# Optimization experiments

Measured on AMD Instinct MI355X. Metric: run time of the kernel, lower is better.

Reference implementation:

```python
import jax, jax.numpy as jnp
import numpy as np

B_G = 16        # number of point clouds
N_PER = 32768   # points per cloud (equal -> no padding)
T = B_G * N_PER
CIN = 16
D = 32          # global_dim
H = 4           # num_heads
HD = D // H
L = 2           # layers
EPS_LN = 1e-5
EPS_Z = 1e-6


def setup_inputs() -> dict:
    key = jax.random.key(0)
    ks = jax.random.split(key, 32)
    r = lambda i, shape, s: (jax.random.normal(ks[i], shape, dtype=jnp.float32) * s)
    inp = {
        "x": r(0, (T, CIN), 1.0),
        "pos": r(1, (T, 3), 1.0),
        "batch": (jnp.arange(T, dtype=jnp.int32) // N_PER),
        "w_in": r(2, (CIN, D), CIN ** -0.5),
        "b_in": r(3, (D,), 0.02),
        "w_pos": r(4, (3, D), 3 ** -0.5),
        "b_pos": r(5, (D,), 0.02),
        "wq": r(6, (L, D, D), D ** -0.5),
        "bq": r(7, (L, D), 0.02),
        "wk": r(8, (L, D, D), D ** -0.5),
        "bk": r(9, (L, D), 0.02),
        "wv": r(10, (L, D, D), D ** -0.5),
        "bv": r(11, (L, D), 0.02),
        "wo": r(12, (L, D, D), D ** -0.5),
        "bo": r(13, (L, D), 0.02),
        "g1": jnp.ones((L, D), jnp.float32),
        "be1": jnp.zeros((L, D), jnp.float32),
        "w1": r(14, (L, D, 2 * D), D ** -0.5),
        "bf1": r(15, (L, 2 * D), 0.02),
        "w2": r(16, (L, 2 * D, D), (2 * D) ** -0.5),
        "bf2": r(17, (L, D), 0.02),
        "g2": jnp.ones((L, D), jnp.float32),
        "be2": jnp.zeros((L, D), jnp.float32),
    }
    return inp


def _layernorm(h, g, b):
    mu = jnp.mean(h, axis=-1, keepdims=True)
    var = jnp.mean(jnp.square(h - mu), axis=-1, keepdims=True)
    return (h - mu) * jax.lax.rsqrt(var + EPS_LN) * g + b


def _linear_attn(h, wq, bq, wk, bk, wv, bv, wo, bo):
    B, N, C = h.shape
    def heads(w, b):
        return (h @ w + b).reshape(B, N, H, HD).transpose(0, 2, 1, 3)  # [B,H,N,hd]
    q = jax.nn.elu(heads(wq, bq)) + 1.0   # ELU feature map phi(.)
    k = jax.nn.elu(heads(wk, bk)) + 1.0
    v = heads(wv, bv)
    kv = jnp.einsum("bhnd,bhne->bhde", k, v)            # O(N) KV summary
    ksum = k.sum(axis=2)                                   # [B,H,hd]
    z = 1.0 / (jnp.einsum("bhnd,bhd->bhn", q, ksum) + EPS_Z)
    out = jnp.einsum("bhnd,bhde->bhne", q, kv) * z[..., None]
    out = out.transpose(0, 2, 1, 3).reshape(B, N, C)
    return out @ wo + bo


def reference(x, pos, batch, w_in, b_in, w_pos, b_pos, wq, bq, wk, bk, wv, bv,
              wo, bo, g1, be1, w1, bf1, w2, bf2, g2, be2):
    # to_dense_batch: batch is sorted; compute per-point index within its segment
    counts = jax.ops.segment_sum(jnp.ones((T,), jnp.int32), batch, num_segments=B_G)
    starts = jnp.concatenate([jnp.zeros((1,), jnp.int32), jnp.cumsum(counts)[:-1]])
    idx = jnp.arange(T, dtype=jnp.int32) - starts[batch]
    x_dense = jnp.zeros((B_G, N_PER, CIN), x.dtype).at[batch, idx].set(x)
    pos_dense = jnp.zeros((B_G, N_PER, 3), pos.dtype).at[batch, idx].set(pos)

    h = (x_dense @ w_in + b_in) + (pos_dense @ w_pos + b_pos)  # [B,N,D]
    for l in range(L):
        h = _layernorm(h + _linear_attn(h, wq[l], bq[l], wk[l], bk[l],
                                        wv[l], bv[l], wo[l], bo[l]), g1[l], be1[l])
        ffn = jax.nn.relu(h @ w1[l] + bf1[l]) @ w2[l] + bf2[l]
        h = _layernorm(h + ffn, g2[l], be2[l])
    return h[batch, idx]  # back to [T, D] (h[mask])
```

## Files before the change

### kernel.cpp

```cpp
#include <hip/hip_runtime.h>

#define KVSZ 288
#define EPS_LN 1e-5f
#define EPS_Z  1e-6f

typedef __attribute__((ext_vector_type(8))) short bf16x8;
typedef __attribute__((ext_vector_type(4))) float f32x4;

#define MFMA(a, b, c) __builtin_amdgcn_mfma_f32_16x16x32_bf16(a, b, c, 0, 0, 0)

#define PWE 0
#define LBASE(l) (1024 + (l) * 8192)
#define PQ 0
#define PO 1024
#define P1 2048
#define P2 4096
#define PK 6144
#define PV 7168

__device__ __forceinline__ unsigned short f2bf(float f) {
  union { float f; unsigned u; } x; x.f = f;
  unsigned r = x.u + 0x7fff + ((x.u >> 16) & 1);
  return (unsigned short)(r >> 16);
}

__device__ __forceinline__ unsigned pkbf(float a, float b) {
#if __has_builtin(__builtin_amdgcn_cvt_pk_bf16_f32)
  typedef __attribute__((ext_vector_type(2))) __bf16 bf16x2_t;
  bf16x2_t v = __builtin_amdgcn_cvt_pk_bf16_f32(a, b);
  return __builtin_bit_cast(unsigned, v);
#else
  return (unsigned)f2bf(a) | ((unsigned)f2bf(b) << 16);
#endif
}

__device__ __forceinline__ float bfu(unsigned short s) {
  union { float f; unsigned u; } x; x.u = ((unsigned)s) << 16; return x.f;
}

__device__ __forceinline__ void lds_fence() { asm volatile("s_waitcnt lgkmcnt(0)" ::: "memory"); }
__device__ __forceinline__ float phi(float x) { return x > 0.f ? x + 1.f : __expf(x); }

__device__ __forceinline__ int perm32(int kp) {
  return ((kp & 4) << 2) | (((kp >> 3) << 2) + (kp & 3));
}

__device__ __forceinline__ bf16x8 bbuild(f32x4 lo, f32x4 hi) {
  union { bf16x8 v; unsigned u[4]; } cv;
  cv.u[0] = pkbf(lo[0], lo[1]); cv.u[1] = pkbf(lo[2], lo[3]);
  cv.u[2] = pkbf(hi[0], hi[1]); cv.u[3] = pkbf(hi[2], hi[3]);
  return cv.v;
}

__device__ __forceinline__ void stage_a32(unsigned short* dst, const float* __restrict__ W,
                                          int N, int tid) {
  for (int i = tid; i < 32 * N; i += 256) {
    int n = i >> 5, kp = i & 31;
    dst[i] = f2bf(W[perm32(kp) * N + n]);
  }
}
__device__ __forceinline__ void stage_a64(unsigned short* dst, const float* __restrict__ W,
                                          int tid) {
  for (int i = tid; i < 64 * 32; i += 256) {
    int n = i >> 6, kp = i & 63;
    int kl = ((kp >> 5) << 5) + perm32(kp & 31);
    dst[i] = f2bf(W[kl * 32 + n]);
  }
}

__device__ __forceinline__ void make_kvm(bf16x8& A0, bf16x8& A1,
                                         const float* __restrict__ kvg,
                                         int quad, int m) {
  union { bf16x8 v; unsigned short s[8]; unsigned u[4]; } a, b;
  a.u[0] = a.u[1] = a.u[2] = a.u[3] = 0u;
  b.u[0] = b.u[1] = b.u[2] = b.u[3] = 0u;
  if ((quad >> 1) == (m >> 3)) {
    int h0 = m >> 3, e7 = m & 7, dq = (quad & 1) * 4;
    const float* p0 = kvg + h0 * 64 + dq * 8 + e7;
    const float* p1 = kvg + (2 + h0) * 64 + dq * 8 + e7;
    a.s[0] = f2bf(p0[0]);  a.s[1] = f2bf(p0[8]);
    a.s[2] = f2bf(p0[16]); a.s[3] = f2bf(p0[24]);
    b.s[4] = f2bf(p1[0]);  b.s[5] = f2bf(p1[8]);
    b.s[6] = f2bf(p1[16]); b.s[7] = f2bf(p1[24]);
  }
  A0 = a.v; A1 = b.v;
}

__device__ __forceinline__ void ln_t(f32x4& a0, f32x4& a1, float4 g0, float4 g1,
                                     float4 b0, float4 b1) {
  float s = a0[0] + a0[1] + a0[2] + a0[3] + a1[0] + a1[1] + a1[2] + a1[3];
  s += __shfl_xor(s, 16); s += __shfl_xor(s, 32);
  float mu = s * (1.f / 32.f);
  float vv = 0.f;
#pragma unroll
  for (int r = 0; r < 4; r++) {
    a0[r] -= mu; a1[r] -= mu;
    vv += a0[r] * a0[r] + a1[r] * a1[r];
  }
  vv += __shfl_xor(vv, 16); vv += __shfl_xor(vv, 32);
  float rstd = rsqrtf(vv * (1.f / 32.f) + EPS_LN);
  a0[0] = a0[0] * rstd * g0.x + b0.x; a0[1] = a0[1] * rstd * g0.y + b0.y;
  a0[2] = a0[2] * rstd * g0.z + b0.z; a0[3] = a0[3] * rstd * g0.w + b0.w;
  a1[0] = a1[0] * rstd * g1.x + b1.x; a1[1] = a1[1] * rstd * g1.y + b1.y;
  a1[2] = a1[2] * rstd * g1.z + b1.z; a1[3] = a1[3] * rstd * g1.w + b1.w;
}

__device__ __forceinline__ void layer_core_g(
    f32x4 (&hc0)[4], f32x4 (&hc1)[4], const unsigned short* __restrict__ pwl,
    const float* __restrict__ kvg, int quad, int m,
    const float* __restrict__ bq, const float* __restrict__ bo,
    const float* __restrict__ g1, const float* __restrict__ be1,
    const float* __restrict__ bf1, const float* __restrict__ bf2,
    const float* __restrict__ g2, const float* __restrict__ be2) {
  const int k0 = quad * 8, q4 = quad * 4;
  {
    const bf16x8 wqA0 = *(const bf16x8*)(pwl + PQ + m * 32 + k0);
    const bf16x8 wqA1 = *(const bf16x8*)(pwl + PQ + (16 + m) * 32 + k0);
    const bf16x8 woA0 = *(const bf16x8*)(pwl + PO + m * 32 + k0);
    const bf16x8 woA1 = *(const bf16x8*)(pwl + PO + (16 + m) * 32 + k0);
    bf16x8 kvA0, kvA1;
    make_kvm(kvA0, kvA1, kvg, quad, m);
    const float4 bq0 = *(const float4*)(bq + q4), bq1 = *(const float4*)(bq + 16 + q4);
    const float4 bo0 = *(const float4*)(bo + q4), bo1 = *(const float4*)(bo + 16 + q4);
    const float4 g10 = *(const float4*)(g1 + q4), g11 = *(const float4*)(g1 + 16 + q4);
    const float4 e10 = *(const float4*)(be1 + q4), e11 = *(const float4*)(be1 + 16 + q4);
    const float4 ks0 = *(const float4*)(kvg + 256 + q4);
    const float4 ks1 = *(const float4*)(kvg + 272 + q4);
#pragma unroll
    for (int mt = 0; mt < 4; mt++) {
      bf16x8 hB = bbuild(hc0[mt], hc1[mt]);
      f32x4 q0 = {bq0.x, bq0.y, bq0.z, bq0.w};
      f32x4 q1 = {bq1.x, bq1.y, bq1.z, bq1.w};
      q0 = MFMA(wqA0, hB, q0);
      q1 = MFMA(wqA1, hB, q1);
#pragma unroll
      for (int r = 0; r < 4; r++) { q0[r] = phi(q0[r]); q1[r] = phi(q1[r]); }
      bf16x8 qB = bbuild(q0, q1);
      f32x4 zz = {0.f, 0.f, 0.f, 0.f};
      f32x4 at0 = MFMA(kvA0, qB, zz);
      f32x4 at1 = MFMA(kvA1, qB, zz);
      float p0 = q0[0] * ks0.x + q0[1] * ks0.y + q0[2] * ks0.z + q0[3] * ks0.w;
      float p1 = q1[0] * ks1.x + q1[1] * ks1.y + q1[2] * ks1.z + q1[3] * ks1.w;
      p0 += __shfl_xor(p0, 16);
      p1 += __shfl_xor(p1, 16);
      float z0 = 1.f / (p0 + EPS_Z), z1 = 1.f / (p1 + EPS_Z);
      bf16x8 aB;
      {
        union { bf16x8 v; unsigned u[4]; } cv;
        cv.u[0] = pkbf(at0[0] * z0, at0[1] * z0); cv.u[1] = pkbf(at0[2] * z0, at0[3] * z0);
        cv.u[2] = pkbf(at1[0] * z1, at1[1] * z1); cv.u[3] = pkbf(at1[2] * z1, at1[3] * z1);
        aB = cv.v;
      }
      f32x4 h0 = hc0[mt], h1 = hc1[mt];
      h0[0] += bo0.x; h0[1] += bo0.y; h0[2] += bo0.z; h0[3] += bo0.w;
      h1[0] += bo1.x; h1[1] += bo1.y; h1[2] += bo1.z; h1[3] += bo1.w;
      h0 = MFMA(woA0, aB, h0);
      h1 = MFMA(woA1, aB, h1);
      ln_t(h0, h1, g10, g11, e10, e11);
      hc0[mt] = h0; hc1[mt] = h1;
    }
  }
  {
    bf16x8 w1A[4]; float4 b1f[4];
#pragma unroll
    for (int nt = 0; nt < 4; nt++) {
      w1A[nt] = *(const bf16x8*)(pwl + P1 + (nt * 16 + m) * 32 + k0);
      b1f[nt] = *(const float4*)(bf1 + nt * 16 + q4);
    }
    const bf16x8 w2L0 = *(const bf16x8*)(pwl + P2 + m * 64 + k0);
    const bf16x8 w2H0 = *(const bf16x8*)(pwl + P2 + m * 64 + 32 + k0);
    const bf16x8 w2L1 = *(const bf16x8*)(pwl + P2 + (16 + m) * 64 + k0);
    const bf16x8 w2H1 = *(const bf16x8*)(pwl + P2 + (16 + m) * 64 + 32 + k0);
    const float4 b20 = *(const float4*)(bf2 + q4), b21 = *(const float4*)(bf2 + 16 + q4);
    const float4 g20 = *(const float4*)(g2 + q4), g21 = *(const float4*)(g2 + 16 + q4);
    const float4 e20 = *(const float4*)(be2 + q4), e21 = *(const float4*)(be2 + 16 + q4);
#pragma unroll
    for (int mt = 0; mt < 4; mt++) {
      bf16x8 hB = bbuild(hc0[mt], hc1[mt]);
      f32x4 hd[4];
#pragma unroll
      for (int nt = 0; nt < 4; nt++) {
        f32x4 ini = {b1f[nt].x, b1f[nt].y, b1f[nt].z, b1f[nt].w};
        hd[nt] = MFMA(w1A[nt], hB, ini);
#pragma unroll
        for (int r = 0; r < 4; r++) hd[nt][r] = fmaxf(hd[nt][r], 0.f);
      }
      bf16x8 fL = bbuild(hd[0], hd[1]);
      bf16x8 fH = bbuild(hd[2], hd[3]);
      f32x4 o0 = hc0[mt], o1 = hc1[mt];
      o0[0] += b20.x; o0[1] += b20.y; o0[2] += b20.z; o0[3] += b20.w;
      o1[0] += b21.x; o1[1] += b21.y; o1[2] += b21.z; o1[3] += b21.w;
      o0 = MFMA(w2L0, fL, o0);
      o0 = MFMA(w2H0, fH, o0);
      o1 = MFMA(w2L1, fL, o1);
      o1 = MFMA(w2H1, fH, o1);
      ln_t(o0, o1, g20, g21, e20, e21);
      hc0[mt] = o0; hc1[mt] = o1;
    }
  }
}

__device__ __forceinline__ void kv_stage_g(
    const f32x4 (&hc0)[4], const f32x4 (&hc1)[4], unsigned short* tw,
    const unsigned short* __restrict__ pwk, const unsigned short* __restrict__ pwv,
    float* blk, int quad, int m,
    const float* __restrict__ bk, const float* __restrict__ bv) {
  const int k0 = quad * 8, q4 = quad * 4;
  unsigned short* Tk = tw;
  unsigned short* Tv = tw + 1280;
  const bf16x8 wkA0 = *(const bf16x8*)(pwk + m * 32 + k0);
  const bf16x8 wkA1 = *(const bf16x8*)(pwk + (16 + m) * 32 + k0);
  const bf16x8 wvA0 = *(const bf16x8*)(pwv + m * 32 + k0);
  const bf16x8 wvA1 = *(const bf16x8*)(pwv + (16 + m) * 32 + k0);
  const float4 bk0 = *(const float4*)(bk + q4), bk1 = *(const float4*)(bk + 16 + q4);
  const float4 bv0 = *(const float4*)(bv + q4), bv1 = *(const float4*)(bv + 16 + q4);
  f32x4 accA = {0.f, 0.f, 0.f, 0.f}, accB = {0.f, 0.f, 0.f, 0.f};
  f32x4 ksa0 = {0.f, 0.f, 0.f, 0.f}, ksa1 = {0.f, 0.f, 0.f, 0.f};
#pragma unroll
  for (int ch = 0; ch < 2; ch++) {
#pragma unroll
    for (int mtl = 0; mtl < 2; mtl++) {
      int mt = ch * 2 + mtl;
      bf16x8 hB = bbuild(hc0[mt], hc1[mt]);
      f32x4 kn0 = {bk0.x, bk0.y, bk0.z, bk0.w};
      f32x4 kn1 = {bk1.x, bk1.y, bk1.z, bk1.w};
      f32x4 vn0 = {bv0.x, bv0.y, bv0.z, bv0.w};
      f32x4 vn1 = {bv1.x, bv1.y, bv1.z, bv1.w};
      kn0 = MFMA(wkA0, hB, kn0);
      kn1 = MFMA(wkA1, hB, kn1);
      vn0 = MFMA(wvA0, hB, vn0);
      vn1 = MFMA(wvA1, hB, vn1);
      int cb = mtl * 16 + m;
#pragma unroll
      for (int r = 0; r < 4; r++) {
        kn0[r] = phi(kn0[r]); kn1[r] = phi(kn1[r]);
        ksa0[r] += kn0[r];    ksa1[r] += kn1[r];
        Tk[(q4 + r) * 40 + cb]      = f2bf(kn0[r]);
        Tk[(16 + q4 + r) * 40 + cb] = f2bf(kn1[r]);
        Tv[(q4 + r) * 40 + cb]      = f2bf(vn0[r]);
        Tv[(16 + q4 + r) * 40 + cb] = f2bf(vn1[r]);
      }
    }
    lds_fence();
    bf16x8 akL = *(const bf16x8*)(Tk + m * 40 + k0);
    bf16x8 akH = *(const bf16x8*)(Tk + (16 + m) * 40 + k0);
    bf16x8 avL = *(const bf16x8*)(Tv + m * 40 + k0);
    bf16x8 avH = *(const bf16x8*)(Tv + (16 + m) * 40 + k0);
    accA = MFMA(akL, avL, accA);
    accB = MFMA(akH, avH, accB);
    lds_fence();
  }
#pragma unroll
  for (int r = 0; r < 4; r++) {
    float v0 = ksa0[r], v1 = ksa1[r];
    v0 += __shfl_xor(v0, 1); v0 += __shfl_xor(v0, 2); v0 += __shfl_xor(v0, 4); v0 += __shfl_xor(v0, 8);
    v1 += __shfl_xor(v1, 1); v1 += __shfl_xor(v1, 2); v1 += __shfl_xor(v1, 4); v1 += __shfl_xor(v1, 8);
    if (m == 0) {
      atomicAdd(&blk[256 + q4 + r], v0);
      atomicAdd(&blk[272 + q4 + r], v1);
    }
  }
  if ((quad >> 1) == (m >> 3)) {
    int h0 = quad >> 1, h1 = 2 + (quad >> 1), e = m & 7;
#pragma unroll
    for (int r = 0; r < 4; r++) {
      int d = (q4 + r) & 7;
      atomicAdd(&blk[h0 * 64 + d * 8 + e], accA[r]);
      atomicAdd(&blk[h1 * 64 + d * 8 + e], accB[r]);
    }
  }
}

__global__ __launch_bounds__(256) void k_prep(
    const float* __restrict__ w_in, const float* __restrict__ w_pos,
    const float* __restrict__ wq, const float* __restrict__ wk,
    const float* __restrict__ wv, const float* __restrict__ wo,
    const float* __restrict__ w1, const float* __restrict__ w2,
    unsigned short* __restrict__ pw) {
  const int tid = threadIdx.x;
  for (int i = tid; i < 1024; i += 256) {
    int n = i >> 5, k = i & 31;
    float v = k < 16 ? w_in[k * 32 + n] : (k < 19 ? w_pos[(k - 16) * 32 + n] : 0.f);
    pw[PWE + i] = f2bf(v);
  }
  for (int l = 0; l < 2; l++) {
    unsigned short* b = pw + LBASE(l);
    stage_a32(b + PQ, wq + l * 1024, 32, tid);
    stage_a32(b + PO, wo + l * 1024, 32, tid);
    stage_a32(b + P1, w1 + l * 2048, 64, tid);
    stage_a64(b + P2, w2 + l * 2048, tid);
    stage_a32(b + PK, wk + l * 1024, 32, tid);
    stage_a32(b + PV, wv + l * 1024, 32, tid);
  }
}

template <int H16>
__global__ __launch_bounds__(256) void k_embed(
    const float* __restrict__ x, const float* __restrict__ pos,
    const float* __restrict__ b_in, const float* __restrict__ b_pos,
    const float* __restrict__ bk, const float* __restrict__ bv,
    const unsigned short* __restrict__ pw, unsigned short* __restrict__ hb,
    float* __restrict__ hf, float* __restrict__ gkv) {
  __shared__ __align__(16) unsigned short tiles[4 * 2560];
  __shared__ float blk[KVSZ];
  const int tid = threadIdx.x;
  const int wv_ = tid >> 6, lane = tid & 63, quad = lane >> 4, m = lane & 15;
  unsigned short* tw = tiles + wv_ * 2560;
  const int cloud = blockIdx.x >> 7;
  const int wbase = blockIdx.x * 256 + wv_ * 64;
  const int k0 = quad * 8, q4 = quad * 4;
  for (int i = tid; i < KVSZ; i += 256) blk[i] = 0.f;
  __syncthreads();
  const bf16x8 weA0 = *(const bf16x8*)(pw + PWE + m * 32 + k0);
  const bf16x8 weA1 = *(const bf16x8*)(pw + PWE + (16 + m) * 32 + k0);
  float4 bi0, bi1;
  {
    float4 a = *(const float4*)(b_in + q4), b = *(const float4*)(b_pos + q4);
    bi0 = make_float4(a.x + b.x, a.y + b.y, a.z + b.z, a.w + b.w);
    float4 c = *(const float4*)(b_in + 16 + q4), d = *(const float4*)(b_pos + 16 + q4);
    bi1 = make_float4(c.x + d.x, c.y + d.y, c.z + d.z, c.w + d.w);
  }
  f32x4 hc0[4], hc1[4];
#pragma unroll
  for (int mt = 0; mt < 4; mt++) {
    int p = wbase + mt * 16 + m;
    union { bf16x8 v; unsigned u[4]; } xb;
    xb.u[0] = xb.u[1] = xb.u[2] = xb.u[3] = 0;
    if (quad < 2) {
      const float4* xp = (const float4*)(x + (size_t)p * 16 + quad * 8);
      float4 t0 = xp[0], t1 = xp[1];
      xb.u[0] = pkbf(t0.x, t0.y); xb.u[1] = pkbf(t0.z, t0.w);
      xb.u[2] = pkbf(t1.x, t1.y); xb.u[3] = pkbf(t1.z, t1.w);
    } else if (quad == 2) {
      const float* pp = pos + (size_t)p * 3;
      xb.u[0] = pkbf(pp[0], pp[1]); xb.u[1] = pkbf(pp[2], 0.f);
    }
    f32x4 i0 = {bi0.x, bi0.y, bi0.z, bi0.w};
    f32x4 i1 = {bi1.x, bi1.y, bi1.z, bi1.w};
    hc0[mt] = MFMA(weA0, xb.v, i0);
    hc1[mt] = MFMA(weA1, xb.v, i1);
    if (H16) {
      *(bf16x8*)(hb + ((size_t)p * 32 + quad * 8)) = bbuild(hc0[mt], hc1[mt]);
    } else {
      float* hp = hf + (size_t)p * 32;
      *(float4*)(hp + q4)      = make_float4(hc0[mt][0], hc0[mt][1], hc0[mt][2], hc0[mt][3]);
      *(float4*)(hp + 16 + q4) = make_float4(hc1[mt][0], hc1[mt][1], hc1[mt][2], hc1[mt][3]);
    }
  }
  kv_stage_g(hc0, hc1, tw, pw + LBASE(0) + PK, pw + LBASE(0) + PV, blk, quad, m, bk, bv);
  __syncthreads();
  float* g = gkv + cloud * KVSZ;
  for (int i = tid; i < KVSZ; i += 256) atomicAdd(&g[i], blk[i]);
}

template <int H16>
__global__ __launch_bounds__(256) void k_mid(
    const float* __restrict__ bq, const float* __restrict__ bo,
    const float* __restrict__ g1, const float* __restrict__ be1,
    const float* __restrict__ bf1, const float* __restrict__ bf2,
    const float* __restrict__ g2, const float* __restrict__ be2,
    const float* __restrict__ bkn, const float* __restrict__ bvn,
    const unsigned short* __restrict__ pw, const float* __restrict__ kv_in,
    float* __restrict__ gkv_out, unsigned short* __restrict__ hb,
    float* __restrict__ hf) {
  __shared__ __align__(16) unsigned short tiles[4 * 2560];
  __shared__ float blk[KVSZ];
  const int tid = threadIdx.x;
  const int wv_ = tid >> 6, lane = tid & 63, quad = lane >> 4, m = lane & 15;
  unsigned short* tw = tiles + wv_ * 2560;
  const int cloud = blockIdx.x >> 7;
  const int wbase = blockIdx.x * 256 + wv_ * 64;
  const int q4 = quad * 4;
  for (int i = tid; i < KVSZ; i += 256) blk[i] = 0.f;
  __syncthreads();
  f32x4 hc0[4], hc1[4];
#pragma unroll
  for (int mt = 0; mt < 4; mt++) {
    int p = wbase + mt * 16 + m;
    if (H16) {
      bf16x8 hv = *(const bf16x8*)(hb + ((size_t)p * 32 + quad * 8));
#pragma unroll
      for (int r = 0; r < 4; r++) {
        hc0[mt][r] = bfu((unsigned short)hv[r]);
        hc1[mt][r] = bfu((unsigned short)hv[4 + r]);
      }
    } else {
      const float* hp = hf + (size_t)p * 32;
      float4 lo = *(const float4*)(hp + q4);
      float4 hi = *(const float4*)(hp + 16 + q4);
      hc0[mt][0] = lo.x; hc0[mt][1] = lo.y; hc0[mt][2] = lo.z; hc0[mt][3] = lo.w;
      hc1[mt][0] = hi.x; hc1[mt][1] = hi.y; hc1[mt][2] = hi.z; hc1[mt][3] = hi.w;
    }
  }
  layer_core_g(hc0, hc1, pw + LBASE(0), kv_in + cloud * KVSZ, quad, m,
               bq, bo, g1, be1, bf1, bf2, g2, be2);
#pragma unroll
  for (int mt = 0; mt < 4; mt++) {
    int p = wbase + mt * 16 + m;
    if (H16) {
      *(bf16x8*)(hb + ((size_t)p * 32 + quad * 8)) = bbuild(hc0[mt], hc1[mt]);
    } else {
      float* hp = hf + (size_t)p * 32;
      *(float4*)(hp + q4)      = make_float4(hc0[mt][0], hc0[mt][1], hc0[mt][2], hc0[mt][3]);
      *(float4*)(hp + 16 + q4) = make_float4(hc1[mt][0], hc1[mt][1], hc1[mt][2], hc1[mt][3]);
    }
  }
  kv_stage_g(hc0, hc1, tw, pw + LBASE(1) + PK, pw + LBASE(1) + PV, blk, quad, m,
             bkn, bvn);
  __syncthreads();
  float* g = gkv_out + cloud * KVSZ;
  for (int i = tid; i < KVSZ; i += 256) atomicAdd(&g[i], blk[i]);
}

template <int H16>
__global__ __launch_bounds__(256) void k_last(
    const float* __restrict__ bq, const float* __restrict__ bo,
    const float* __restrict__ g1, const float* __restrict__ be1,
    const float* __restrict__ bf1, const float* __restrict__ bf2,
    const float* __restrict__ g2, const float* __restrict__ be2,
    const unsigned short* __restrict__ pw, const float* __restrict__ kv_in,
    const unsigned short* __restrict__ hb, float* __restrict__ out) {
  const int tid = threadIdx.x;
  const int wv_ = tid >> 6, lane = tid & 63, quad = lane >> 4, m = lane & 15;
  const int cloud = blockIdx.x >> 7;
  const int wbase = blockIdx.x * 256 + wv_ * 64;
  const int q4 = quad * 4;
  f32x4 hc0[4], hc1[4];
#pragma unroll
  for (int mt = 0; mt < 4; mt++) {
    int p = wbase + mt * 16 + m;
    if (H16) {
      bf16x8 hv = *(const bf16x8*)(hb + ((size_t)p * 32 + quad * 8));
#pragma unroll
      for (int r = 0; r < 4; r++) {
        hc0[mt][r] = bfu((unsigned short)hv[r]);
        hc1[mt][r] = bfu((unsigned short)hv[4 + r]);
      }
    } else {
      const float* hp = out + (size_t)p * 32;
      float4 lo = *(const float4*)(hp + q4);
      float4 hi = *(const float4*)(hp + 16 + q4);
      hc0[mt][0] = lo.x; hc0[mt][1] = lo.y; hc0[mt][2] = lo.z; hc0[mt][3] = lo.w;
      hc1[mt][0] = hi.x; hc1[mt][1] = hi.y; hc1[mt][2] = hi.z; hc1[mt][3] = hi.w;
    }
  }
  layer_core_g(hc0, hc1, pw + LBASE(1), kv_in + cloud * KVSZ, quad, m,
               bq, bo, g1, be1, bf1, bf2, g2, be2);
#pragma unroll
  for (int mt = 0; mt < 4; mt++) {
    int p = wbase + mt * 16 + m;
    float* hp = out + (size_t)p * 32;
    *(float4*)(hp + q4)      = make_float4(hc0[mt][0], hc0[mt][1], hc0[mt][2], hc0[mt][3]);
    *(float4*)(hp + 16 + q4) = make_float4(hc1[mt][0], hc1[mt][1], hc1[mt][2], hc1[mt][3]);
  }
}

extern "C" void kernel_launch(void* const* d_in, const int* in_sizes, int n_in,
                              void* d_out, int out_size, void* d_ws, size_t ws_size,
                              hipStream_t stream) {
  (void)in_sizes; (void)n_in; (void)out_size;
  const float* x     = (const float*)d_in[0];
  const float* pos   = (const float*)d_in[1];
  const float* w_in  = (const float*)d_in[3];
  const float* b_in  = (const float*)d_in[4];
  const float* w_pos = (const float*)d_in[5];
  const float* b_pos = (const float*)d_in[6];
  const float* wq  = (const float*)d_in[7];
  const float* bq  = (const float*)d_in[8];
  const float* wk  = (const float*)d_in[9];
  const float* bk  = (const float*)d_in[10];
  const float* wv  = (const float*)d_in[11];
  const float* bv  = (const float*)d_in[12];
  const float* wo  = (const float*)d_in[13];
  const float* bo  = (const float*)d_in[14];
  const float* g1  = (const float*)d_in[15];
  const float* be1 = (const float*)d_in[16];
  const float* w1  = (const float*)d_in[17];
  const float* bf1 = (const float*)d_in[18];
  const float* w2  = (const float*)d_in[19];
  const float* bf2 = (const float*)d_in[20];
  const float* g2  = (const float*)d_in[21];
  const float* be2 = (const float*)d_in[22];
  float* out = (float*)d_out;
  float* kvbuf = (float*)d_ws;
  unsigned short* pw = (unsigned short*)((char*)d_ws + 40960);
  unsigned short* hb = (unsigned short*)((char*)d_ws + 131072);
  const size_t need = 131072ull + 524288ull * 32ull * 2ull;
  const bool h16 = ws_size >= need;

  hipMemsetAsync(kvbuf, 0, 2 * 16 * KVSZ * sizeof(float), stream);
  k_prep<<<dim3(1), dim3(256), 0, stream>>>(w_in, w_pos, wq, wk, wv, wo, w1, w2, pw);
  dim3 grid(2048), block(256);
  if (h16) {
    k_embed<1><<<grid, block, 0, stream>>>(x, pos, b_in, b_pos, bk, bv, pw, hb, out, kvbuf);
    k_mid<1><<<grid, block, 0, stream>>>(bq, bo, g1, be1, bf1, bf2, g2, be2,
                                         bk + 32, bv + 32, pw, kvbuf,
                                         kvbuf + 16 * KVSZ, hb, out);
    k_last<1><<<grid, block, 0, stream>>>(bq + 32, bo + 32, g1 + 32, be1 + 32,
                                          bf1 + 64, bf2 + 32, g2 + 32, be2 + 32,
                                          pw, kvbuf + 16 * KVSZ, hb, out);
  } else {
    k_embed<0><<<grid, block, 0, stream>>>(x, pos, b_in, b_pos, bk, bv, pw, hb, out, kvbuf);
    k_mid<0><<<grid, block, 0, stream>>>(bq, bo, g1, be1, bf1, bf2, g2, be2,
                                         bk + 32, bv + 32, pw, kvbuf,
                                         kvbuf + 16 * KVSZ, hb, out);
    k_last<0><<<grid, block, 0, stream>>>(bq + 32, bo + 32, g1 + 32, be1 + 32,
                                          bf1 + 64, bf2 + 32, g2 + 32, be2 + 32,
                                          pw, kvbuf + 16 * KVSZ, hb, out);
  }
}
```

Before: 267.2 us.

## Stage layer weights and block-diagonal KV matrix in LDS, reuse bf16 fragments

Each block now copies the bf16 layer weights, the KV summary matrix (built once per block as a block-diagonal bf16 tile) and the k-sum vector into shared memory. Per-lane MFMA operands are then read from LDS instead of global memory, and the per-lane make_kvm construction is removed. The bf16 h fragments are also kept and reused for the Q/K/V MFMAs rather than rebuilt from fp32. The cost is extra LDS per block, which may lower occupancy, plus one cooperative staging pass and a sync at the start of each block.

```diff
diff --git a/kernel.cpp b/kernel.cpp
--- a/kernel.cpp
+++ b/kernel.cpp
@@ -68,22 +68,14 @@
   }
 }
 
-__device__ __forceinline__ void make_kvm(bf16x8& A0, bf16x8& A1,
-                                         const float* __restrict__ kvg,
-                                         int quad, int m) {
-  union { bf16x8 v; unsigned short s[8]; unsigned u[4]; } a, b;
-  a.u[0] = a.u[1] = a.u[2] = a.u[3] = 0u;
-  b.u[0] = b.u[1] = b.u[2] = b.u[3] = 0u;
-  if ((quad >> 1) == (m >> 3)) {
-    int h0 = m >> 3, e7 = m & 7, dq = (quad & 1) * 4;
-    const float* p0 = kvg + h0 * 64 + dq * 8 + e7;
-    const float* p1 = kvg + (2 + h0) * 64 + dq * 8 + e7;
-    a.s[0] = f2bf(p0[0]);  a.s[1] = f2bf(p0[8]);
-    a.s[2] = f2bf(p0[16]); a.s[3] = f2bf(p0[24]);
-    b.s[4] = f2bf(p1[0]);  b.s[5] = f2bf(p1[8]);
-    b.s[6] = f2bf(p1[16]); b.s[7] = f2bf(p1[24]);
-  }
-  A0 = a.v; A1 = b.v;
+__device__ __forceinline__ void stage_kvm_lds(unsigned short* dst,
+                                              const float* __restrict__ kvg, int tid) {
+  for (int i = tid; i < 1024; i += 256) {
+    int e = i >> 5, kp = i & 31;
+    int d = perm32(kp);
+    float v = ((d >> 3) == (e >> 3)) ? kvg[(e >> 3) * 64 + (d & 7) * 8 + (e & 7)] : 0.f;
+    dst[i] = f2bf(v);
+  }
 }
 
 __device__ __forceinline__ void ln_t(f32x4& a0, f32x4& a1, float4 g0, float4 g1,
@@ -105,34 +97,34 @@
   a1[2] = a1[2] * rstd * g1.z + b1.z; a1[3] = a1[3] * rstd * g1.w + b1.w;
 }
 
-__device__ __forceinline__ void layer_core_g(
-    f32x4 (&hc0)[4], f32x4 (&hc1)[4], const unsigned short* __restrict__ pwl,
-    const float* __restrict__ kvg, int quad, int m,
+__device__ __forceinline__ void layer_core_l(
+    f32x4 (&hc0)[4], f32x4 (&hc1)[4], const bf16x8 (&hBp)[4],
+    const unsigned short* lw, const unsigned short* kvm, const float* kss,
+    int quad, int m,
     const float* __restrict__ bq, const float* __restrict__ bo,
     const float* __restrict__ g1, const float* __restrict__ be1,
     const float* __restrict__ bf1, const float* __restrict__ bf2,
     const float* __restrict__ g2, const float* __restrict__ be2) {
   const int k0 = quad * 8, q4 = quad * 4;
   {
-    const bf16x8 wqA0 = *(const bf16x8*)(pwl + PQ + m * 32 + k0);
-    const bf16x8 wqA1 = *(const bf16x8*)(pwl + PQ + (16 + m) * 32 + k0);
-    const bf16x8 woA0 = *(const bf16x8*)(pwl + PO + m * 32 + k0);
-    const bf16x8 woA1 = *(const bf16x8*)(pwl + PO + (16 + m) * 32 + k0);
-    bf16x8 kvA0, kvA1;
-    make_kvm(kvA0, kvA1, kvg, quad, m);
+    const bf16x8 wqA0 = *(const bf16x8*)(lw + PQ + m * 32 + k0);
+    const bf16x8 wqA1 = *(const bf16x8*)(lw + PQ + (16 + m) * 32 + k0);
+    const bf16x8 woA0 = *(const bf16x8*)(lw + PO + m * 32 + k0);
+    const bf16x8 woA1 = *(const bf16x8*)(lw + PO + (16 + m) * 32 + k0);
+    const bf16x8 kvA0 = *(const bf16x8*)(kvm + m * 32 + k0);
+    const bf16x8 kvA1 = *(const bf16x8*)(kvm + (16 + m) * 32 + k0);
     const float4 bq0 = *(const float4*)(bq + q4), bq1 = *(const float4*)(bq + 16 + q4);
     const float4 bo0 = *(const float4*)(bo + q4), bo1 = *(const float4*)(bo + 16 + q4);
     const float4 g10 = *(const float4*)(g1 + q4), g11 = *(const float4*)(g1 + 16 + q4);
     const float4 e10 = *(const float4*)(be1 + q4), e11 = *(const float4*)(be1 + 16 + q4);
-    const float4 ks0 = *(const float4*)(kvg + 256 + q4);
-    const float4 ks1 = *(const float4*)(kvg + 272 + q4);
+    const float4 ks0 = *(const float4*)(kss + q4);
+    const float4 ks1 = *(const float4*)(kss + 16 + q4);
 #pragma unroll
     for (int mt = 0; mt < 4; mt++) {
-      bf16x8 hB = bbuild(hc0[mt], hc1[mt]);
       f32x4 q0 = {bq0.x, bq0.y, bq0.z, bq0.w};
       f32x4 q1 = {bq1.x, bq1.y, bq1.z, bq1.w};
-      q0 = MFMA(wqA0, hB, q0);
-      q1 = MFMA(wqA1, hB, q1);
+      q0 = MFMA(wqA0, hBp[mt], q0);
+      q1 = MFMA(wqA1, hBp[mt], q1);
 #pragma unroll
       for (int r = 0; r < 4; r++) { q0[r] = phi(q0[r]); q1[r] = phi(q1[r]); }
       bf16x8 qB = bbuild(q0, q1);
@@ -164,13 +156,13 @@
     bf16x8 w1A[4]; float4 b1f[4];
 #pragma unroll
     for (int nt = 0; nt < 4; nt++) {
-      w1A[nt] = *(const bf16x8*)(pwl + P1 + (nt * 16 + m) * 32 + k0);
+      w1A[nt] = *(const bf16x8*)(lw + P1 + (nt * 16 + m) * 32 + k0);
       b1f[nt] = *(const float4*)(bf1 + nt * 16 + q4);
     }
-    const bf16x8 w2L0 = *(const bf16x8*)(pwl + P2 + m * 64 + k0);
-    const bf16x8 w2H0 = *(const bf16x8*)(pwl + P2 + m * 64 + 32 + k0);
-    const bf16x8 w2L1 = *(const bf16x8*)(pwl + P2 + (16 + m) * 64 + k0);
-    const bf16x8 w2H1 = *(const bf16x8*)(pwl + P2 + (16 + m) * 64 + 32 + k0);
+    const bf16x8 w2L0 = *(const bf16x8*)(lw + P2 + m * 64 + k0);
+    const bf16x8 w2H0 = *(const bf16x8*)(lw + P2 + m * 64 + 32 + k0);
+    const bf16x8 w2L1 = *(const bf16x8*)(lw + P2 + (16 + m) * 64 + k0);
+    const bf16x8 w2H1 = *(const bf16x8*)(lw + P2 + (16 + m) * 64 + 32 + k0);
     const float4 b20 = *(const float4*)(bf2 + q4), b21 = *(const float4*)(bf2 + 16 + q4);
     const float4 g20 = *(const float4*)(g2 + q4), g21 = *(const float4*)(g2 + 16 + q4);
     const float4 e20 = *(const float4*)(be2 + q4), e21 = *(const float4*)(be2 + 16 + q4);
@@ -200,18 +192,18 @@
   }
 }
 
-__device__ __forceinline__ void kv_stage_g(
-    const f32x4 (&hc0)[4], const f32x4 (&hc1)[4], unsigned short* tw,
-    const unsigned short* __restrict__ pwk, const unsigned short* __restrict__ pwv,
+__device__ __forceinline__ void kv_stage_l(
+    const bf16x8 (&hBp)[4], unsigned short* tw,
+    const unsigned short* lwK, const unsigned short* lwV,
     float* blk, int quad, int m,
     const float* __restrict__ bk, const float* __restrict__ bv) {
   const int k0 = quad * 8, q4 = quad * 4;
   unsigned short* Tk = tw;
   unsigned short* Tv = tw + 1280;
-  const bf16x8 wkA0 = *(const bf16x8*)(pwk + m * 32 + k0);
-  const bf16x8 wkA1 = *(const bf16x8*)(pwk + (16 + m) * 32 + k0);
-  const bf16x8 wvA0 = *(const bf16x8*)(pwv + m * 32 + k0);
-  const bf16x8 wvA1 = *(const bf16x8*)(pwv + (16 + m) * 32 + k0);
+  const bf16x8 wkA0 = *(const bf16x8*)(lwK + m * 32 + k0);
+  const bf16x8 wkA1 = *(const bf16x8*)(lwK + (16 + m) * 32 + k0);
+  const bf16x8 wvA0 = *(const bf16x8*)(lwV + m * 32 + k0);
+  const bf16x8 wvA1 = *(const bf16x8*)(lwV + (16 + m) * 32 + k0);
   const float4 bk0 = *(const float4*)(bk + q4), bk1 = *(const float4*)(bk + 16 + q4);
   const float4 bv0 = *(const float4*)(bv + q4), bv1 = *(const float4*)(bv + 16 + q4);
   f32x4 accA = {0.f, 0.f, 0.f, 0.f}, accB = {0.f, 0.f, 0.f, 0.f};
@@ -221,15 +213,14 @@
 #pragma unroll
     for (int mtl = 0; mtl < 2; mtl++) {
       int mt = ch * 2 + mtl;
-      bf16x8 hB = bbuild(hc0[mt], hc1[mt]);
       f32x4 kn0 = {bk0.x, bk0.y, bk0.z, bk0.w};
       f32x4 kn1 = {bk1.x, bk1.y, bk1.z, bk1.w};
       f32x4 vn0 = {bv0.x, bv0.y, bv0.z, bv0.w};
       f32x4 vn1 = {bv1.x, bv1.y, bv1.z, bv1.w};
-      kn0 = MFMA(wkA0, hB, kn0);
-      kn1 = MFMA(wkA1, hB, kn1);
-      vn0 = MFMA(wvA0, hB, vn0);
-      vn1 = MFMA(wvA1, hB, vn1);
+      kn0 = MFMA(wkA0, hBp[mt], kn0);
+      kn1 = MFMA(wkA1, hBp[mt], kn1);
+      vn0 = MFMA(wvA0, hBp[mt], vn0);
+      vn1 = MFMA(wvA1, hBp[mt], vn1);
       int cb = mtl * 16 + m;
 #pragma unroll
       for (int r = 0; r < 4; r++) {
@@ -301,6 +292,7 @@
     const float* __restrict__ bk, const float* __restrict__ bv,
     const unsigned short* __restrict__ pw, unsigned short* __restrict__ hb,
     float* __restrict__ hf, float* __restrict__ gkv) {
+  __shared__ __align__(16) unsigned short lws[3072];
   __shared__ __align__(16) unsigned short tiles[4 * 2560];
   __shared__ float blk[KVSZ];
   const int tid = threadIdx.x;
@@ -309,10 +301,16 @@
   const int cloud = blockIdx.x >> 7;
   const int wbase = blockIdx.x * 256 + wv_ * 64;
   const int k0 = quad * 8, q4 = quad * 4;
+  for (int j = tid; j < 384; j += 256) {
+    int i = j * 8;
+    const unsigned short* src = (i < 1024) ? (pw + PWE + i)
+                                           : (pw + LBASE(0) + PK + (i - 1024));
+    *(bf16x8*)(lws + i) = *(const bf16x8*)src;
+  }
   for (int i = tid; i < KVSZ; i += 256) blk[i] = 0.f;
   __syncthreads();
-  const bf16x8 weA0 = *(const bf16x8*)(pw + PWE + m * 32 + k0);
-  const bf16x8 weA1 = *(const bf16x8*)(pw + PWE + (16 + m) * 32 + k0);
+  const bf16x8 weA0 = *(const bf16x8*)(lws + m * 32 + k0);
+  const bf16x8 weA1 = *(const bf16x8*)(lws + (16 + m) * 32 + k0);
   float4 bi0, bi1;
   {
     float4 a = *(const float4*)(b_in + q4), b = *(const float4*)(b_pos + q4);
@@ -320,7 +318,7 @@
     float4 c = *(const float4*)(b_in + 16 + q4), d = *(const float4*)(b_pos + 16 + q4);
     bi1 = make_float4(c.x + d.x, c.y + d.y, c.z + d.z, c.w + d.w);
   }
-  f32x4 hc0[4], hc1[4];
+  bf16x8 fr[4];
 #pragma unroll
   for (int mt = 0; mt < 4; mt++) {
     int p = wbase + mt * 16 + m;
@@ -337,17 +335,18 @@
     }
     f32x4 i0 = {bi0.x, bi0.y, bi0.z, bi0.w};
     f32x4 i1 = {bi1.x, bi1.y, bi1.z, bi1.w};
-    hc0[mt] = MFMA(weA0, xb.v, i0);
-    hc1[mt] = MFMA(weA1, xb.v, i1);
+    f32x4 h0 = MFMA(weA0, xb.v, i0);
+    f32x4 h1 = MFMA(weA1, xb.v, i1);
+    fr[mt] = bbuild(h0, h1);
     if (H16) {
-      *(bf16x8*)(hb + ((size_t)p * 32 + quad * 8)) = bbuild(hc0[mt], hc1[mt]);
+      *(bf16x8*)(hb + ((size_t)p * 32 + quad * 8)) = fr[mt];
     } else {
       float* hp = hf + (size_t)p * 32;
-      *(float4*)(hp + q4)      = make_float4(hc0[mt][0], hc0[mt][1], hc0[mt][2], hc0[mt][3]);
-      *(float4*)(hp + 16 + q4) = make_float4(hc1[mt][0], hc1[mt][1], hc1[mt][2], hc1[mt][3]);
-    }
-  }
-  kv_stage_g(hc0, hc1, tw, pw + LBASE(0) + PK, pw + LBASE(0) + PV, blk, quad, m, bk, bv);
+      *(float4*)(hp + q4)      = make_float4(h0[0], h0[1], h0[2], h0[3]);
+      *(float4*)(hp + 16 + q4) = make_float4(h1[0], h1[1], h1[2], h1[3]);
+    }
+  }
+  kv_stage_l(fr, tw, lws + 1024, lws + 2048, blk, quad, m, bk, bv);
   __syncthreads();
   float* g = gkv + cloud * KVSZ;
   for (int i = tid; i < KVSZ; i += 256) atomicAdd(&g[i], blk[i]);
@@ -363,6 +362,9 @@
     const unsigned short* __restrict__ pw, const float* __restrict__ kv_in,
     float* __restrict__ gkv_out, unsigned short* __restrict__ hb,
     float* __restrict__ hf) {
+  __shared__ __align__(16) unsigned short lws[8192];
+  __shared__ __align__(16) unsigned short kvm[1024];
+  __shared__ __align__(16) float kss[32];
   __shared__ __align__(16) unsigned short tiles[4 * 2560];
   __shared__ float blk[KVSZ];
   const int tid = threadIdx.x;
@@ -371,18 +373,28 @@
   const int cloud = blockIdx.x >> 7;
   const int wbase = blockIdx.x * 256 + wv_ * 64;
   const int q4 = quad * 4;
+  const float* kvg = kv_in + cloud * KVSZ;
+  for (int j = tid; j < 1024; j += 256) {
+    int i = j * 8;
+    const unsigned short* src = (i < 6144) ? (pw + LBASE(0) + i)
+                                           : (pw + LBASE(1) + PK + (i - 6144));
+    *(bf16x8*)(lws + i) = *(const bf16x8*)src;
+  }
+  stage_kvm_lds(kvm, kvg, tid);
+  if (tid < 32) kss[tid] = kvg[256 + tid];
   for (int i = tid; i < KVSZ; i += 256) blk[i] = 0.f;
   __syncthreads();
   f32x4 hc0[4], hc1[4];
+  bf16x8 fr[4];
 #pragma unroll
   for (int mt = 0; mt < 4; mt++) {
     int p = wbase + mt * 16 + m;
     if (H16) {
-      bf16x8 hv = *(const bf16x8*)(hb + ((size_t)p * 32 + quad * 8));
+      fr[mt] = *(const bf16x8*)(hb + ((size_t)p * 32 + quad * 8));
 #pragma unroll
       for (int r = 0; r < 4; r++) {
-        hc0[mt][r] = bfu((unsigned short)hv[r]);
-        hc1[mt][r] = bfu((unsigned short)hv[4 + r]);
+        hc0[mt][r] = bfu((unsigned short)fr[mt][r]);
+        hc1[mt][r] = bfu((unsigned short)fr[mt][4 + r]);
       }
     } else {
       const float* hp = hf + (size_t)p * 32;
@@ -390,23 +402,24 @@
       float4 hi = *(const float4*)(hp + 16 + q4);
       hc0[mt][0] = lo.x; hc0[mt][1] = lo.y; hc0[mt][2] = lo.z; hc0[mt][3] = lo.w;
       hc1[mt][0] = hi.x; hc1[mt][1] = hi.y; hc1[mt][2] = hi.z; hc1[mt][3] = hi.w;
-    }
-  }
-  layer_core_g(hc0, hc1, pw + LBASE(0), kv_in + cloud * KVSZ, quad, m,
+      fr[mt] = bbuild(hc0[mt], hc1[mt]);
+    }
+  }
+  layer_core_l(hc0, hc1, fr, lws, kvm, kss, quad, m,
                bq, bo, g1, be1, bf1, bf2, g2, be2);
 #pragma unroll
   for (int mt = 0; mt < 4; mt++) {
     int p = wbase + mt * 16 + m;
+    fr[mt] = bbuild(hc0[mt], hc1[mt]);
     if (H16) {
-      *(bf16x8*)(hb + ((size_t)p * 32 + quad * 8)) = bbuild(hc0[mt], hc1[mt]);
+      *(bf16x8*)(hb + ((size_t)p * 32 + quad * 8)) = fr[mt];
     } else {
       float* hp = hf + (size_t)p * 32;
       *(float4*)(hp + q4)      = make_float4(hc0[mt][0], hc0[mt][1], hc0[mt][2], hc0[mt][3]);
       *(float4*)(hp + 16 + q4) = make_float4(hc1[mt][0], hc1[mt][1], hc1[mt][2], hc1[mt][3]);
     }
   }
-  kv_stage_g(hc0, hc1, tw, pw + LBASE(1) + PK, pw + LBASE(1) + PV, blk, quad, m,
-             bkn, bvn);
+  kv_stage_l(fr, tw, lws + 6144, lws + 7168, blk, quad, m, bkn, bvn);
   __syncthreads();
   float* g = gkv_out + cloud * KVSZ;
   for (int i = tid; i < KVSZ; i += 256) atomicAdd(&g[i], blk[i]);
@@ -420,21 +433,31 @@
     const float* __restrict__ g2, const float* __restrict__ be2,
     const unsigned short* __restrict__ pw, const float* __restrict__ kv_in,
     const unsigned short* __restrict__ hb, float* __restrict__ out) {
+  __shared__ __align__(16) unsigned short lws[6144];
+  __shared__ __align__(16) unsigned short kvm[1024];
+  __shared__ __align__(16) float kss[32];
   const int tid = threadIdx.x;
   const int wv_ = tid >> 6, lane = tid & 63, quad = lane >> 4, m = lane & 15;
   const int cloud = blockIdx.x >> 7;
   const int wbase = blockIdx.x * 256 + wv_ * 64;
   const int q4 = quad * 4;
+  const float* kvg = kv_in + cloud * KVSZ;
+  for (int j = tid; j < 768; j += 256)
+    *(bf16x8*)(lws + j * 8) = *(const bf16x8*)(pw + LBASE(1) + j * 8);
+  stage_kvm_lds(kvm, kvg, tid);
+  if (tid < 32) kss[tid] = kvg[256 + tid];
+  __syncthreads();
   f32x4 hc0[4], hc1[4];
+  bf16x8 fr[4];
 #pragma unroll
   for (int mt = 0; mt < 4; mt++) {
     int p = wbase + mt * 16 + m;
     if (H16) {
-      bf16x8 hv = *(const bf16x8*)(hb + ((size_t)p * 32 + quad * 8));
+      fr[mt] = *(const bf16x8*)(hb + ((size_t)p * 32 + quad * 8));
 #pragma unroll
       for (int r = 0; r < 4; r++) {
-        hc0[mt][r] = bfu((unsigned short)hv[r]);
-        hc1[mt][r] = bfu((unsigned short)hv[4 + r]);
+        hc0[mt][r] = bfu((unsigned short)fr[mt][r]);
+        hc1[mt][r] = bfu((unsigned short)fr[mt][4 + r]);
       }
     } else {
       const float* hp = out + (size_t)p * 32;
@@ -442,9 +465,10 @@
       float4 hi = *(const float4*)(hp + 16 + q4);
       hc0[mt][0] = lo.x; hc0[mt][1] = lo.y; hc0[mt][2] = lo.z; hc0[mt][3] = lo.w;
       hc1[mt][0] = hi.x; hc1[mt][1] = hi.y; hc1[mt][2] = hi.z; hc1[mt][3] = hi.w;
-    }
-  }
-  layer_core_g(hc0, hc1, pw + LBASE(1), kv_in + cloud * KVSZ, quad, m,
+      fr[mt] = bbuild(hc0[mt], hc1[mt]);
+    }
+  }
+  layer_core_l(hc0, hc1, fr, lws, kvm, kss, quad, m,
                bq, bo, g1, be1, bf1, bf2, g2, be2);
 #pragma unroll
   for (int mt = 0; mt < 4; mt++) {
```

Measured after the change: 256.8 us. 3.9% less time.
